# Performance work log

Hardware: AMD Instinct MI355X
Metric: run time of the kernel (lower is better)

Reference implementation:

```python
import jax, jax.numpy as jnp
import numpy as np

D_MODEL = 768
N_HEAD = 12
HEAD_DIM = D_MODEL // N_HEAD
SCALE = HEAD_DIM ** -0.5
B, T = 8, 1024
NEG_INF = -1e9


def setup_inputs() -> dict:
    key = jax.random.key(0)
    ks = jax.random.split(key, 4)
    x = jax.random.normal(ks[0], (B, T, D_MODEL), dtype=jnp.float32)
    W_attn = jax.random.normal(ks[1], (D_MODEL, 3 * D_MODEL), dtype=jnp.float32) * 0.02
    b_attn = jnp.zeros((3 * D_MODEL,), dtype=jnp.float32)
    W_proj = jax.random.normal(ks[2], (D_MODEL, D_MODEL), dtype=jnp.float32) * 0.02
    b_proj = jnp.zeros((D_MODEL,), dtype=jnp.float32)
    return {"x": x, "W_attn": W_attn, "b_attn": b_attn, "W_proj": W_proj, "b_proj": b_proj}


def reference(x, W_attn, b_attn, W_proj, b_proj):
    Bn, Tn, C = x.shape
    # fused QKV projection: [B,T,3C]
    qkv = jnp.einsum('btc,cd->btd', x, W_attn) + b_attn
    q, k, v = jnp.split(qkv, 3, axis=-1)
    # [B, H, T, hd]
    def heads(t):
        return t.reshape(Bn, Tn, N_HEAD, HEAD_DIM).transpose(0, 2, 1, 3)
    q, k, v = heads(q), heads(k), heads(v)
    # scaled dot-product scores [B,H,T,T]
    att = jnp.einsum('bhqd,bhkd->bhqk', q, k) * SCALE
    # causal mask: mask[i,j]=1 where j>i (upper triangle, excluded)
    causal = jnp.tril(jnp.ones((Tn, Tn), dtype=bool))
    att = jnp.where(causal[None, None, :, :], att, NEG_INF)
    att = jax.nn.softmax(att, axis=-1)
    # weighted value sum -> merge heads
    y = jnp.einsum('bhqk,bhkd->bhqd', att, v)
    y = y.transpose(0, 2, 1, 3).reshape(Bn, Tn, C)
    # output projection
    return jnp.einsum('btc,cd->btd', y, W_proj) + b_proj
```

## Files before the change

### kernel.cpp

```cpp
#include <hip/hip_runtime.h>
#include <hip/hip_bf16.h>

#define T_SEQ 1024
#define NBATCH 8
#define NHEAD 12
#define HD 64
#define CDIM 768
#define C3 2304

typedef __attribute__((ext_vector_type(8))) __bf16 bf16x8;
typedef __attribute__((ext_vector_type(4))) __bf16 bf16x4;
typedef __attribute__((ext_vector_type(2))) __bf16 bf16x2;
typedef __attribute__((ext_vector_type(4))) float  f32x4;
typedef __attribute__((ext_vector_type(16))) float f32x16;

__device__ __forceinline__ f32x4 mfma_bf16(bf16x8 a, bf16x8 b, f32x4 c) {
    return __builtin_amdgcn_mfma_f32_16x16x32_bf16(a, b, c, 0, 0, 0);
}
__device__ __forceinline__ f32x16 mfma32(bf16x8 a, bf16x8 b, f32x16 c) {
    return __builtin_amdgcn_mfma_f32_32x32x16_bf16(a, b, c, 0, 0, 0);
}

__device__ __forceinline__ void gload16(const void* g, void* l) {
    __builtin_amdgcn_global_load_lds(
        (const __attribute__((address_space(1))) unsigned int*)g,
        (__attribute__((address_space(3))) unsigned int*)l, 16, 0, 0);
}

#define WAIT_VM(N)  asm volatile("s_waitcnt vmcnt(" #N ")" ::: "memory")
#define WAIT_LGKM0  asm volatile("s_waitcnt lgkmcnt(0)" ::: "memory")

__global__ __launch_bounds__(256) void prep(const float* __restrict__ x,
                                            __bf16* __restrict__ xb,
                                            const float* __restrict__ Wa,
                                            __bf16* __restrict__ Wat,
                                            const float* __restrict__ Wp,
                                            __bf16* __restrict__ Wpt) {
    __shared__ float tile[32][33];
    const int bx = blockIdx.x;
    if (bx < 6144) {
        int i = bx * 256 + threadIdx.x;
        float4 v = ((const float4*)x)[i];
        bf16x4 o = { (__bf16)v.x, (__bf16)v.y, (__bf16)v.z, (__bf16)v.w };
        ((bf16x4*)xb)[i] = o;
        return;
    }
    const int b2 = bx - 6144;
    const int gx = b2 % 96, gy = b2 / 96;
    const float* W;  __bf16* Wt;  int C, c0;
    if (gx < 72) { W = Wa; Wt = Wat; C = 2304; c0 = gx * 32; }
    else         { W = Wp; Wt = Wpt; C = 768;  c0 = (gx - 72) * 32; }
    const int r0 = gy * 32;
    const int tc = threadIdx.x & 31, tr = threadIdx.x >> 5;
#pragma unroll
    for (int i = 0; i < 4; ++i)
        tile[tr + i * 8][tc] = W[(size_t)(r0 + tr + i * 8) * C + c0 + tc];
    __syncthreads();
#pragma unroll
    for (int i = 0; i < 4; ++i)
        Wt[(size_t)(c0 + tr + i * 8) * 768 + r0 + tc] = (__bf16)tile[tc][tr + i * 8];
}

__global__ __launch_bounds__(256) void gemm_qkv(const __bf16* __restrict__ A,
                                                const __bf16* __restrict__ Bt,
                                                const float* __restrict__ bias,
                                                __bf16* __restrict__ Cout,
                                                int M, int N, int K) {
    __shared__ __align__(16) __bf16 sA[3][128 * 32];
    __shared__ __align__(16) __bf16 sB[3][128 * 32];
    const int t = threadIdx.x, l = t & 63, w = t >> 6;
    const int l31 = l & 31, lh = l >> 5;
    const int wr = w >> 1, wc = w & 1;
    const int xcd = blockIdx.x & 7;
    const int local = blockIdx.x >> 3;
    const int m0 = (xcd * 8 + (local & 7)) * 128;
    const int n0 = (local >> 3) * 128;

    const int r_st = t >> 2;
    const int sw_st = (r_st & 3) ^ ((r_st >> 2) & 3);
    const int g_off = ((t & 3) ^ sw_st) << 3;
    const int sw_rd = (l31 & 3) ^ ((l31 >> 2) & 3);

    f32x16 acc[2][2];
#pragma unroll
    for (int m = 0; m < 2; ++m)
#pragma unroll
        for (int n = 0; n < 2; ++n)
#pragma unroll
            for (int r = 0; r < 16; ++r) acc[m][n][r] = 0.f;

    const int nk = K >> 5;

#pragma unroll
    for (int s = 0; s < 3; ++s) {
        const int k0 = s << 5;
#pragma unroll
        for (int i = 0; i < 2; ++i) {
            int r = i * 64 + r_st;
            gload16(A + (size_t)(m0 + r) * K + k0 + g_off,
                    (char*)&sA[s][0] + (i * 256 + w * 64) * 16);
            gload16(Bt + (size_t)(n0 + r) * K + k0 + g_off,
                    (char*)&sB[s][0] + (i * 256 + w * 64) * 16);
        }
    }

    int cur = 0;
    for (int kt = 0; kt < nk; ++kt) {
        if (kt + 2 < nk)      WAIT_VM(8);
        else if (kt + 1 < nk) WAIT_VM(4);
        else                  WAIT_VM(0);
        __builtin_amdgcn_s_barrier();

        bf16x8 af[2][2], bg[2][2];
#pragma unroll
        for (int m = 0; m < 2; ++m)
#pragma unroll
            for (int ks = 0; ks < 2; ++ks)
                af[m][ks] = *(const bf16x8*)(&sA[cur][(wr * 64 + m * 32 + l31) * 32
                                                      + ((((ks << 1) | lh) ^ sw_rd) << 3)]);
#pragma unroll
        for (int n = 0; n < 2; ++n)
#pragma unroll
            for (int ks = 0; ks < 2; ++ks)
                bg[n][ks] = *(const bf16x8*)(&sB[cur][(wc * 64 + n * 32 + l31) * 32
                                                      + ((((ks << 1) | lh) ^ sw_rd) << 3)]);

#pragma unroll
        for (int ks = 0; ks < 2; ++ks)
#pragma unroll
            for (int m = 0; m < 2; ++m)
#pragma unroll
                for (int n = 0; n < 2; ++n)
                    acc[m][n] = mfma32(af[m][ks], bg[n][ks], acc[m][n]);

        WAIT_LGKM0;
        __builtin_amdgcn_s_barrier();

        if (kt + 3 < nk) {
            const int k0 = (kt + 3) << 5;
#pragma unroll
            for (int i = 0; i < 2; ++i) {
                int r = i * 64 + r_st;
                gload16(A + (size_t)(m0 + r) * K + k0 + g_off,
                        (char*)&sA[cur][0] + (i * 256 + w * 64) * 16);
                gload16(Bt + (size_t)(n0 + r) * K + k0 + g_off,
                        (char*)&sB[cur][0] + (i * 256 + w * 64) * 16);
            }
        }
        cur = (cur == 2) ? 0 : cur + 1;
    }

#pragma unroll
    for (int n = 0; n < 2; ++n) {
        int col = n0 + wc * 64 + n * 32 + l31;
        float bv = bias[col];
#pragma unroll
        for (int m = 0; m < 2; ++m) {
            int rbase = m0 + wr * 64 + m * 32 + 4 * lh;
#pragma unroll
            for (int r = 0; r < 16; ++r) {
                int row = rbase + (r & 3) + 8 * (r >> 2);
                Cout[(size_t)row * N + col] = (__bf16)(acc[m][n][r] + bv);
            }
        }
    }
}

__global__ __launch_bounds__(256) void gemm_proj(const __bf16* __restrict__ A,
                                                 const __bf16* __restrict__ Bt,
                                                 const float* __restrict__ bias,
                                                 float* __restrict__ Cout,
                                                 int M, int N, int K) {
    __shared__ __align__(16) __bf16 sA[3][64 * 32];
    __shared__ __align__(16) __bf16 sB[3][128 * 32];
    const int t = threadIdx.x, l = t & 63, w = t >> 6;
    const int l31 = l & 31, lh = l >> 5;
    const int wr = w >> 1, wc = w & 1;
    const int xcd = blockIdx.x & 7;
    const int local = blockIdx.x >> 3;
    const int m0 = (xcd * 16 + (local & 15)) * 64;
    const int n0 = (local >> 4) * 128;

    const int r_st = t >> 2;
    const int sw_st = (r_st & 3) ^ ((r_st >> 2) & 3);
    const int g_off = ((t & 3) ^ sw_st) << 3;
    const int sw_rd = (l31 & 3) ^ ((l31 >> 2) & 3);

    f32x16 acc[2];
#pragma unroll
    for (int n = 0; n < 2; ++n)
#pragma unroll
        for (int r = 0; r < 16; ++r) acc[n][r] = 0.f;

    const int nk = K >> 5;

#pragma unroll
    for (int s = 0; s < 3; ++s) {
        const int k0 = s << 5;
        gload16(A + (size_t)(m0 + r_st) * K + k0 + g_off,
                (char*)&sA[s][0] + (w * 64) * 16);
#pragma unroll
        for (int i = 0; i < 2; ++i)
            gload16(Bt + (size_t)(n0 + i * 64 + r_st) * K + k0 + g_off,
                    (char*)&sB[s][0] + (i * 256 + w * 64) * 16);
    }

    int cur = 0;
    for (int kt = 0; kt < nk; ++kt) {
        if (kt + 2 < nk)      WAIT_VM(6);
        else if (kt + 1 < nk) WAIT_VM(3);
        else                  WAIT_VM(0);
        __builtin_amdgcn_s_barrier();

        bf16x8 af[2], bg[2][2];
#pragma unroll
        for (int ks = 0; ks < 2; ++ks)
            af[ks] = *(const bf16x8*)(&sA[cur][(wr * 32 + l31) * 32
                                              + ((((ks << 1) | lh) ^ sw_rd) << 3)]);
#pragma unroll
        for (int n = 0; n < 2; ++n)
#pragma unroll
            for (int ks = 0; ks < 2; ++ks)
                bg[n][ks] = *(const bf16x8*)(&sB[cur][(wc * 64 + n * 32 + l31) * 32
                                                      + ((((ks << 1) | lh) ^ sw_rd) << 3)]);

#pragma unroll
        for (int ks = 0; ks < 2; ++ks)
#pragma unroll
            for (int n = 0; n < 2; ++n)
                acc[n] = mfma32(af[ks], bg[n][ks], acc[n]);

        WAIT_LGKM0;
        __builtin_amdgcn_s_barrier();

        if (kt + 3 < nk) {
            const int k0 = (kt + 3) << 5;
            gload16(A + (size_t)(m0 + r_st) * K + k0 + g_off,
                    (char*)&sA[cur][0] + (w * 64) * 16);
#pragma unroll
            for (int i = 0; i < 2; ++i)
                gload16(Bt + (size_t)(n0 + i * 64 + r_st) * K + k0 + g_off,
                        (char*)&sB[cur][0] + (i * 256 + w * 64) * 16);
        }
        cur = (cur == 2) ? 0 : cur + 1;
    }

#pragma unroll
    for (int n = 0; n < 2; ++n) {
        int col = n0 + wc * 64 + n * 32 + l31;
        float bv = bias[col];
        int rbase = m0 + wr * 32 + 4 * lh;
#pragma unroll
        for (int r = 0; r < 16; ++r) {
            int row = rbase + (r & 3) + 8 * (r >> 2);
            Cout[(size_t)row * N + col] = acc[n][r] + bv;
        }
    }
}

__global__ __launch_bounds__(256, 2) void attn_fwd(const __bf16* __restrict__ qkv,
                                                   __bf16* __restrict__ y) {
    const int tid = threadIdx.x, l = tid & 63, w = tid >> 6;
    const int lr = l & 15, lk = l >> 4;
    const int r7 = lr & 7;
    const int bid = blockIdx.x;
    const int pr = bid / 96;
    const int hb = bid % 96;
    const int h = hb % NHEAD;
    const int b = hb / NHEAD;

    __shared__ __align__(16) __bf16 sK[2][64][64];
    __shared__ __align__(16) __bf16 sV[2][64][64];
    __shared__ __align__(16) __bf16 sP[4][16][72];

    const size_t baseQ = (size_t)b * T_SEQ * C3 + h * HD;
    const __bf16* Kp = qkv + baseQ + CDIM;
    const __bf16* Vp = qkv + baseQ + 2 * CDIM;

    const int vk0 = tid >> 3;
    const int vc = (tid & 7) << 3;
    const int vg = tid & 7;
    const int krow = tid >> 3;
    const int kchunk = (tid & 7) ^ ((tid >> 3) & 7);

#pragma unroll 1
    for (int job = 0; job < 2; ++job) {
        const int qt = (job == 0) ? pr : 15 - pr;
        const int q0 = qt * 64;
        const int nt = qt + 1;
        const int q_abs = q0 + w * 16 + lr;

        const size_t rowQ = baseQ + (size_t)(q0 + w * 16 + lr) * C3;
        bf16x8 qa0 = *(const bf16x8*)(qkv + rowQ + lk * 8);
        bf16x8 qa1 = *(const bf16x8*)(qkv + rowQ + 32 + lk * 8);
#pragma unroll
        for (int e = 0; e < 8; ++e) {
            qa0[e] = (__bf16)((float)qa0[e] * 0.125f);
            qa1[e] = (__bf16)((float)qa1[e] * 0.125f);
        }

        f32x4 acc[4];
#pragma unroll
        for (int fd = 0; fd < 4; ++fd) acc[fd] = f32x4{0.f, 0.f, 0.f, 0.f};
        float mrun = -1e30f, lrun = 0.f;

        bf16x8 vreg[2];
#pragma unroll
        for (int i = 0; i < 2; ++i)
            vreg[i] = *(const bf16x8*)(Vp + (size_t)(i * 32 + vk0) * C3 + vc);
#pragma unroll
        for (int i = 0; i < 2; ++i)
            gload16(Kp + (size_t)(i * 32 + krow) * C3 + kchunk * 8,
                    (char*)&sK[0][0][0] + (i * 256 + w * 64) * 16);
#pragma unroll
        for (int i = 0; i < 2; ++i) {
            int key = i * 32 + vk0;
#pragma unroll
            for (int e = 0; e < 8; ++e)
                sV[0][vc + e][key ^ ((e ^ vg) << 3)] = vreg[i][e];
        }
        __syncthreads();

#pragma unroll 1
        for (int t = 0; t < nt; ++t) {
            const int kv0 = t * 64;
            const int cur = t & 1, nxt = cur ^ 1;
            const bool pre = (t + 1 < nt);
            if (pre) {
                const int kvp = kv0 + 64;
#pragma unroll
                for (int i = 0; i < 2; ++i)
                    vreg[i] = *(const bf16x8*)(Vp + (size_t)(kvp + i * 32 + vk0) * C3 + vc);
#pragma unroll
                for (int i = 0; i < 2; ++i)
                    gload16(Kp + (size_t)(kvp + i * 32 + krow) * C3 + kchunk * 8,
                            (char*)&sK[nxt][0][0] + (i * 256 + w * 64) * 16);
            }
            f32x4 s[4];
            __builtin_amdgcn_s_setprio(1);
#pragma unroll
            for (int fc = 0; fc < 4; ++fc) {
                const __bf16* kr = &sK[cur][fc * 16 + lr][0];
                bf16x8 k0 = *(const bf16x8*)(kr + ((lk ^ r7) << 3));
                bf16x8 k1 = *(const bf16x8*)(kr + (((4 + lk) ^ r7) << 3));
                f32x4 z = f32x4{0.f, 0.f, 0.f, 0.f};
                z = mfma_bf16(k0, qa0, z);
                z = mfma_bf16(k1, qa1, z);
                s[fc] = z;
            }
            __builtin_amdgcn_s_setprio(0);
            float ps[4][4];
#pragma unroll
            for (int fc = 0; fc < 4; ++fc)
#pragma unroll
                for (int j = 0; j < 4; ++j) ps[fc][j] = s[fc][j];
            if (t == nt - 1) {
#pragma unroll
                for (int fc = 0; fc < 4; ++fc)
#pragma unroll
                    for (int j = 0; j < 4; ++j) {
                        int key = kv0 + fc * 16 + lk * 4 + j;
                        if (key > q_abs) ps[fc][j] = -1e30f;
                    }
            }
            float mfc[4];
#pragma unroll
            for (int fc = 0; fc < 4; ++fc)
                mfc[fc] = fmaxf(fmaxf(ps[fc][0], ps[fc][1]), fmaxf(ps[fc][2], ps[fc][3]));
            float mt = fmaxf(fmaxf(mfc[0], mfc[1]), fmaxf(mfc[2], mfc[3]));
            mt = fmaxf(mt, __shfl_xor(mt, 16, 64));
            mt = fmaxf(mt, __shfl_xor(mt, 32, 64));
            if (!__all(mt - mrun <= 8.f)) {
                const float mn = fmaxf(mrun, mt);
                const float corr = __expf(mrun - mn);
                mrun = mn;
                lrun *= corr;
                float cj[4];
#pragma unroll
                for (int j = 0; j < 4; ++j) cj[j] = __shfl(corr, lk * 4 + j, 64);
#pragma unroll
                for (int fd = 0; fd < 4; ++fd)
#pragma unroll
                    for (int j = 0; j < 4; ++j) acc[fd][j] *= cj[j];
            }
            float rs = 0.f;
#pragma unroll
            for (int fc = 0; fc < 4; ++fc)
#pragma unroll
                for (int j = 0; j < 4; ++j) {
                    float p = __expf(ps[fc][j] - mrun);
                    ps[fc][j] = p;
                    rs += p;
                }
            rs += __shfl_xor(rs, 16, 64);
            rs += __shfl_xor(rs, 32, 64);
            lrun += rs;
#pragma unroll
            for (int fc = 0; fc < 4; ++fc)
#pragma unroll
                for (int jp = 0; jp < 2; ++jp) {
                    bf16x2 pk = { (__bf16)ps[fc][jp * 2], (__bf16)ps[fc][jp * 2 + 1] };
                    *(bf16x2*)&sP[w][lr][fc * 16 + lk * 4 + jp * 2] = pk;
                }
            __builtin_amdgcn_s_setprio(1);
#pragma unroll
            for (int ks = 0; ks < 2; ++ks) {
                bf16x8 pa = *(const bf16x8*)&sP[w][lr][ks * 32 + lk * 8];
#pragma unroll
                for (int fd = 0; fd < 4; ++fd) {
                    int d = fd * 16 + lr;
                    int sw = ((d & 7) ^ ((d >> 3) & 7)) << 3;
                    bf16x8 vb = *(const bf16x8*)&sV[cur][d][(ks * 32 + lk * 8) ^ sw];
                    acc[fd] = mfma_bf16(pa, vb, acc[fd]);
                }
            }
            __builtin_amdgcn_s_setprio(0);
            if (pre) {
#pragma unroll
                for (int i = 0; i < 2; ++i) {
                    int key = i * 32 + vk0;
#pragma unroll
                    for (int e = 0; e < 8; ++e)
                        sV[nxt][vc + e][key ^ ((e ^ vg) << 3)] = vreg[i][e];
                }
            }
            __syncthreads();
        }

        float linv[4];
#pragma unroll
        for (int j = 0; j < 4; ++j) linv[j] = 1.f / __shfl(lrun, lk * 4 + j, 64);
        const size_t yrow0 = (size_t)(b * T_SEQ + q0 + w * 16 + lk * 4);
#pragma unroll
        for (int fd = 0; fd < 4; ++fd) {
            int col = h * HD + fd * 16 + lr;
#pragma unroll
            for (int j = 0; j < 4; ++j)
                y[(yrow0 + j) * CDIM + col] = (__bf16)(acc[fd][j] * linv[j]);
        }
    }
}

extern "C" void kernel_launch(void* const* d_in, const int* in_sizes, int n_in,
                              void* d_out, int out_size, void* d_ws, size_t ws_size,
                              hipStream_t stream) {
    const float* x      = (const float*)d_in[0];
    const float* W_attn = (const float*)d_in[1];
    const float* b_attn = (const float*)d_in[2];
    const float* W_proj = (const float*)d_in[3];
    const float* b_proj = (const float*)d_in[4];

    __bf16* xb  = (__bf16*)d_ws;
    __bf16* Wat = xb  + (size_t)8192 * 768;
    __bf16* Wpt = Wat + (size_t)2304 * 768;
    __bf16* qkv = Wpt + (size_t)768 * 768;
    __bf16* yb  = qkv + (size_t)8192 * 2304;

    prep<<<6144 + 2304, 256, 0, stream>>>(x, xb, W_attn, Wat, W_proj, Wpt);
    gemm_qkv<<<18 * 64, 256, 0, stream>>>(xb, Wat, b_attn, qkv, 8192, 2304, 768);
    attn_fwd<<<NBATCH * NHEAD * 8, 256, 0, stream>>>(qkv, yb);
    gemm_proj<<<768, 256, 0, stream>>>(yb, Wpt, b_proj, (float*)d_out, 8192, 768, 768);
}
```

Baseline: 111.0 us.

## Process both paired causal query tiles in one KV sweep sharing K/V loads

```diff
diff --git a/kernel.cpp b/kernel.cpp
--- a/kernel.cpp
+++ b/kernel.cpp
@@ -283,59 +283,67 @@
     const int krow = tid >> 3;
     const int kchunk = (tid & 7) ^ ((tid >> 3) & 7);
 
+    const int q0A = pr * 64, q0B = (15 - pr) * 64;
+    const int ntB = 16 - pr;
+    const int qA = q0A + w * 16 + lr;
+    const int qB = q0B + w * 16 + lr;
+
+    const size_t rowQA = baseQ + (size_t)(q0A + w * 16 + lr) * C3;
+    const size_t rowQB = baseQ + (size_t)(q0B + w * 16 + lr) * C3;
+    bf16x8 qaA0 = *(const bf16x8*)(qkv + rowQA + lk * 8);
+    bf16x8 qaA1 = *(const bf16x8*)(qkv + rowQA + 32 + lk * 8);
+    bf16x8 qaB0 = *(const bf16x8*)(qkv + rowQB + lk * 8);
+    bf16x8 qaB1 = *(const bf16x8*)(qkv + rowQB + 32 + lk * 8);
+#pragma unroll
+    for (int e = 0; e < 8; ++e) {
+        qaA0[e] = (__bf16)((float)qaA0[e] * 0.125f);
+        qaA1[e] = (__bf16)((float)qaA1[e] * 0.125f);
+        qaB0[e] = (__bf16)((float)qaB0[e] * 0.125f);
+        qaB1[e] = (__bf16)((float)qaB1[e] * 0.125f);
+    }
+
+    f32x4 accA[4], accB[4];
+#pragma unroll
+    for (int fd = 0; fd < 4; ++fd) {
+        accA[fd] = f32x4{0.f, 0.f, 0.f, 0.f};
+        accB[fd] = f32x4{0.f, 0.f, 0.f, 0.f};
+    }
+    float mA = -1e30f, lA = 0.f, mB = -1e30f, lB = 0.f;
+
+    bf16x8 vreg[2];
+#pragma unroll
+    for (int i = 0; i < 2; ++i)
+        vreg[i] = *(const bf16x8*)(Vp + (size_t)(i * 32 + vk0) * C3 + vc);
+#pragma unroll
+    for (int i = 0; i < 2; ++i)
+        gload16(Kp + (size_t)(i * 32 + krow) * C3 + kchunk * 8,
+                (char*)&sK[0][0][0] + (i * 256 + w * 64) * 16);
+#pragma unroll
+    for (int i = 0; i < 2; ++i) {
+        int key = i * 32 + vk0;
+#pragma unroll
+        for (int e = 0; e < 8; ++e)
+            sV[0][vc + e][key ^ ((e ^ vg) << 3)] = vreg[i][e];
+    }
+    __syncthreads();
+
 #pragma unroll 1
-    for (int job = 0; job < 2; ++job) {
-        const int qt = (job == 0) ? pr : 15 - pr;
-        const int q0 = qt * 64;
-        const int nt = qt + 1;
-        const int q_abs = q0 + w * 16 + lr;
-
-        const size_t rowQ = baseQ + (size_t)(q0 + w * 16 + lr) * C3;
-        bf16x8 qa0 = *(const bf16x8*)(qkv + rowQ + lk * 8);
-        bf16x8 qa1 = *(const bf16x8*)(qkv + rowQ + 32 + lk * 8);
-#pragma unroll
-        for (int e = 0; e < 8; ++e) {
-            qa0[e] = (__bf16)((float)qa0[e] * 0.125f);
-            qa1[e] = (__bf16)((float)qa1[e] * 0.125f);
-        }
-
-        f32x4 acc[4];
-#pragma unroll
-        for (int fd = 0; fd < 4; ++fd) acc[fd] = f32x4{0.f, 0.f, 0.f, 0.f};
-        float mrun = -1e30f, lrun = 0.f;
-
-        bf16x8 vreg[2];
-#pragma unroll
-        for (int i = 0; i < 2; ++i)
-            vreg[i] = *(const bf16x8*)(Vp + (size_t)(i * 32 + vk0) * C3 + vc);
-#pragma unroll
-        for (int i = 0; i < 2; ++i)
-            gload16(Kp + (size_t)(i * 32 + krow) * C3 + kchunk * 8,
-                    (char*)&sK[0][0][0] + (i * 256 + w * 64) * 16);
-#pragma unroll
-        for (int i = 0; i < 2; ++i) {
-            int key = i * 32 + vk0;
-#pragma unroll
-            for (int e = 0; e < 8; ++e)
-                sV[0][vc + e][key ^ ((e ^ vg) << 3)] = vreg[i][e];
-        }
-        __syncthreads();
-
-#pragma unroll 1
-        for (int t = 0; t < nt; ++t) {
-            const int kv0 = t * 64;
-            const int cur = t & 1, nxt = cur ^ 1;
-            const bool pre = (t + 1 < nt);
-            if (pre) {
-                const int kvp = kv0 + 64;
-#pragma unroll
-                for (int i = 0; i < 2; ++i)
-                    vreg[i] = *(const bf16x8*)(Vp + (size_t)(kvp + i * 32 + vk0) * C3 + vc);
-#pragma unroll
-                for (int i = 0; i < 2; ++i)
-                    gload16(Kp + (size_t)(kvp + i * 32 + krow) * C3 + kchunk * 8,
-                            (char*)&sK[nxt][0][0] + (i * 256 + w * 64) * 16);
-            }
+    for (int t = 0; t < ntB; ++t) {
+        const int kv0 = t * 64;
+        const int cur = t & 1, nxt = cur ^ 1;
+        const bool pre = (t + 1 < ntB);
+        if (pre) {
+            const int kvp = kv0 + 64;
+#pragma unroll
+            for (int i = 0; i < 2; ++i)
+                vreg[i] = *(const bf16x8*)(Vp + (size_t)(kvp + i * 32 + vk0) * C3 + vc);
+#pragma unroll
+            for (int i = 0; i < 2; ++i)
+                gload16(Kp + (size_t)(kvp + i * 32 + krow) * C3 + kchunk * 8,
+                        (char*)&sK[nxt][0][0] + (i * 256 + w * 64) * 16);
+        }
+
+        {
             f32x4 s[4];
             __builtin_amdgcn_s_setprio(1);
 #pragma unroll
@@ -344,8 +352,8 @@
                 bf16x8 k0 = *(const bf16x8*)(kr + ((lk ^ r7) << 3));
                 bf16x8 k1 = *(const bf16x8*)(kr + (((4 + lk) ^ r7) << 3));
                 f32x4 z = f32x4{0.f, 0.f, 0.f, 0.f};
-                z = mfma_bf16(k0, qa0, z);
-                z = mfma_bf16(k1, qa1, z);
+                z = mfma_bf16(k0, qaB0, z);
+                z = mfma_bf16(k1, qaB1, z);
                 s[fc] = z;
             }
             __builtin_amdgcn_s_setprio(0);
@@ -354,13 +362,13 @@
             for (int fc = 0; fc < 4; ++fc)
 #pragma unroll
                 for (int j = 0; j < 4; ++j) ps[fc][j] = s[fc][j];
-            if (t == nt - 1) {
+            if (t == ntB - 1) {
 #pragma unroll
                 for (int fc = 0; fc < 4; ++fc)
 #pragma unroll
                     for (int j = 0; j < 4; ++j) {
                         int key = kv0 + fc * 16 + lk * 4 + j;
-                        if (key > q_abs) ps[fc][j] = -1e30f;
+                        if (key > qB) ps[fc][j] = -1e30f;
                     }
             }
             float mfc[4];
@@ -370,31 +378,31 @@
             float mt = fmaxf(fmaxf(mfc[0], mfc[1]), fmaxf(mfc[2], mfc[3]));
             mt = fmaxf(mt, __shfl_xor(mt, 16, 64));
             mt = fmaxf(mt, __shfl_xor(mt, 32, 64));
-            if (!__all(mt - mrun <= 8.f)) {
-                const float mn = fmaxf(mrun, mt);
-                const float corr = __expf(mrun - mn);
-                mrun = mn;
-                lrun *= corr;
+            if (!__all(mt - mB <= 8.f)) {
+                const float mn = fmaxf(mB, mt);
+                const float corr = __expf(mB - mn);
+                mB = mn;
+                lB *= corr;
                 float cj[4];
 #pragma unroll
                 for (int j = 0; j < 4; ++j) cj[j] = __shfl(corr, lk * 4 + j, 64);
 #pragma unroll
                 for (int fd = 0; fd < 4; ++fd)
 #pragma unroll
-                    for (int j = 0; j < 4; ++j) acc[fd][j] *= cj[j];
+                    for (int j = 0; j < 4; ++j) accB[fd][j] *= cj[j];
             }
             float rs = 0.f;
 #pragma unroll
             for (int fc = 0; fc < 4; ++fc)
 #pragma unroll
                 for (int j = 0; j < 4; ++j) {
-                    float p = __expf(ps[fc][j] - mrun);
+                    float p = __expf(ps[fc][j] - mB);
                     ps[fc][j] = p;
                     rs += p;
                 }
             rs += __shfl_xor(rs, 16, 64);
             rs += __shfl_xor(rs, 32, 64);
-            lrun += rs;
+            lB += rs;
 #pragma unroll
             for (int fc = 0; fc < 4; ++fc)
 #pragma unroll
@@ -411,32 +419,130 @@
                     int d = fd * 16 + lr;
                     int sw = ((d & 7) ^ ((d >> 3) & 7)) << 3;
                     bf16x8 vb = *(const bf16x8*)&sV[cur][d][(ks * 32 + lk * 8) ^ sw];
-                    acc[fd] = mfma_bf16(pa, vb, acc[fd]);
+                    accB[fd] = mfma_bf16(pa, vb, accB[fd]);
                 }
             }
             __builtin_amdgcn_s_setprio(0);
-            if (pre) {
-#pragma unroll
-                for (int i = 0; i < 2; ++i) {
-                    int key = i * 32 + vk0;
-#pragma unroll
-                    for (int e = 0; e < 8; ++e)
-                        sV[nxt][vc + e][key ^ ((e ^ vg) << 3)] = vreg[i][e];
+        }
+
+        if (t <= pr) {
+            f32x4 s[4];
+            __builtin_amdgcn_s_setprio(1);
+#pragma unroll
+            for (int fc = 0; fc < 4; ++fc) {
+                const __bf16* kr = &sK[cur][fc * 16 + lr][0];
+                bf16x8 k0 = *(const bf16x8*)(kr + ((lk ^ r7) << 3));
+                bf16x8 k1 = *(const bf16x8*)(kr + (((4 + lk) ^ r7) << 3));
+                f32x4 z = f32x4{0.f, 0.f, 0.f, 0.f};
+                z = mfma_bf16(k0, qaA0, z);
+                z = mfma_bf16(k1, qaA1, z);
+                s[fc] = z;
+            }
+            __builtin_amdgcn_s_setprio(0);
+            float ps[4][4];
+#pragma unroll
+            for (int fc = 0; fc < 4; ++fc)
+#pragma unroll
+                for (int j = 0; j < 4; ++j) ps[fc][j] = s[fc][j];
+            if (t == pr) {
+#pragma unroll
+                for (int fc = 0; fc < 4; ++fc)
+#pragma unroll
+                    for (int j = 0; j < 4; ++j) {
+                        int key = kv0 + fc * 16 + lk * 4 + j;
+                        if (key > qA) ps[fc][j] = -1e30f;
+                    }
+            }
+            float mfc[4];
+#pragma unroll
+            for (int fc = 0; fc < 4; ++fc)
+                mfc[fc] = fmaxf(fmaxf(ps[fc][0], ps[fc][1]), fmaxf(ps[fc][2], ps[fc][3]));
+            float mt = fmaxf(fmaxf(mfc[0], mfc[1]), fmaxf(mfc[2], mfc[3]));
+            mt = fmaxf(mt, __shfl_xor(mt, 16, 64));
+            mt = fmaxf(mt, __shfl_xor(mt, 32, 64));
+            if (!__all(mt - mA <= 8.f)) {
+                const float mn = fmaxf(mA, mt);
+                const float corr = __expf(mA - mn);
+                mA = mn;
+                lA *= corr;
+                float cj[4];
+#pragma unroll
+                for (int j = 0; j < 4; ++j) cj[j] = __shfl(corr, lk * 4 + j, 64);
+#pragma unroll
+                for (int fd = 0; fd < 4; ++fd)
+#pragma unroll
+                    for (int j = 0; j < 4; ++j) accA[fd][j] *= cj[j];
+            }
+            float rs = 0.f;
+#pragma unroll
+            for (int fc = 0; fc < 4; ++fc)
+#pragma unroll
+                for (int j = 0; j < 4; ++j) {
+                    float p = __expf(ps[fc][j] - mA);
+                    ps[fc][j] = p;
+                    rs += p;
                 }
-            }
-            __syncthreads();
-        }
-
+            rs += __shfl_xor(rs, 16, 64);
+            rs += __shfl_xor(rs, 32, 64);
+            lA += rs;
+#pragma unroll
+            for (int fc = 0; fc < 4; ++fc)
+#pragma unroll
+                for (int jp = 0; jp < 2; ++jp) {
+                    bf16x2 pk = { (__bf16)ps[fc][jp * 2], (__bf16)ps[fc][jp * 2 + 1] };
+                    *(bf16x2*)&sP[w][lr][fc * 16 + lk * 4 + jp * 2] = pk;
+                }
+            __builtin_amdgcn_s_setprio(1);
+#pragma unroll
+            for (int ks = 0; ks < 2; ++ks) {
+                bf16x8 pa = *(const bf16x8*)&sP[w][lr][ks * 32 + lk * 8];
+#pragma unroll
+                for (int fd = 0; fd < 4; ++fd) {
+                    int d = fd * 16 + lr;
+                    int sw = ((d & 7) ^ ((d >> 3) & 7)) << 3;
+                    bf16x8 vb = *(const bf16x8*)&sV[cur][d][(ks * 32 + lk * 8) ^ sw];
+                    accA[fd] = mfma_bf16(pa, vb, accA[fd]);
+                }
+            }
+            __builtin_amdgcn_s_setprio(0);
+        }
+
+        if (pre) {
+#pragma unroll
+            for (int i = 0; i < 2; ++i) {
+                int key = i * 32 + vk0;
+#pragma unroll
+                for (int e = 0; e < 8; ++e)
+                    sV[nxt][vc + e][key ^ ((e ^ vg) << 3)] = vreg[i][e];
+            }
+        }
+        __syncthreads();
+    }
+
+    {
         float linv[4];
 #pragma unroll
-        for (int j = 0; j < 4; ++j) linv[j] = 1.f / __shfl(lrun, lk * 4 + j, 64);
-        const size_t yrow0 = (size_t)(b * T_SEQ + q0 + w * 16 + lk * 4);
+        for (int j = 0; j < 4; ++j) linv[j] = 1.f / __shfl(lA, lk * 4 + j, 64);
+        const size_t yrow0 = (size_t)(b * T_SEQ + q0A + w * 16 + lk * 4);
 #pragma unroll
         for (int fd = 0; fd < 4; ++fd) {
             int col = h * HD + fd * 16 + lr;
 #pragma unroll
             for (int j = 0; j < 4; ++j)
-                y[(yrow0 + j) * CDIM + col] = (__bf16)(acc[fd][j] * linv[j]);
+                y[(yrow0 + j) * CDIM + col] = (__bf16)(accA[fd][j] * linv[j]);
+        }
+    }
+    {
+        float linv[4];
+#pragma unroll
+        for (int j = 0; j < 4; ++j) linv[j] = 1.f / __shfl(lB, lk * 4 + j, 64);
+        const size_t yrow0 = (size_t)(b * T_SEQ + q0B + w * 16 + lk * 4);
+#pragma unroll
+        for (int fd = 0; fd < 4; ++fd) {
+            int col = h * HD + fd * 16 + lr;
+#pragma unroll
+            for (int j = 0; j < 4; ++j)
+                y[(yrow0 + j) * CDIM + col] = (__bf16)(accB[fd][j] * linv[j]);
         }
     }
 }
```

New measurement: 108.4 us (median of 2 runs). 1.02x faster.
